# Optimization experiments

Measured on AMD Instinct MI355X. Metric: run time of the kernel, lower is better.

The kernel has to match this reference:

```python
import jax, jax.numpy as jnp
import numpy as np

# Gating config (matches init_kwargs)
N_GROUPS = 4        # n_expert_groups
TOPK_GROUPS = 2     # n_limited_groups
TOPK = 4            # n_activated_experts
ROUTE_SCALE = 1.0


def setup_inputs() -> dict:
    key = jax.random.key(0)
    ks = jax.random.split(key, 8)
    T, D, E, I = 2048, 1024, 16, 512
    s = 0.02  # init scale for sane numerics
    return {
        "x": jax.random.normal(ks[0], (T, D), jnp.float32),
        "gate_w": jax.random.normal(ks[1], (E, D), jnp.float32) * s,
        "w1": jax.random.normal(ks[2], (E, I, D), jnp.float32) * s,
        "w2": jax.random.normal(ks[3], (E, D, I), jnp.float32) * s,
        "w3": jax.random.normal(ks[4], (E, I, D), jnp.float32) * s,
        "ws1": jax.random.normal(ks[5], (I, D), jnp.float32) * s,
        "ws2": jax.random.normal(ks[6], (D, I), jnp.float32) * s,
        "ws3": jax.random.normal(ks[7], (I, D), jnp.float32) * s,
    }


def _gate(x, gate_w):
    # GateDeepSeekV3.forward: softmax scores, group-limited routing, top-k experts.
    T = x.shape[0]
    scores = jax.nn.softmax((x @ gate_w.T).astype(jnp.float32), axis=-1)  # [T, E]
    original_scores = scores
    E = scores.shape[-1]
    # group-limited routing: keep top `TOPK_GROUPS` groups by max score (bias is None)
    s = scores.reshape(T, N_GROUPS, E // N_GROUPS)
    group_scores = s.max(axis=-1)                                  # [T, G]
    _, gidx = jax.lax.top_k(group_scores, TOPK_GROUPS)             # [T, Gk]
    mask = jnp.zeros((T, N_GROUPS), scores.dtype).at[jnp.arange(T)[:, None], gidx].set(1.0)
    s = (s * mask[:, :, None]).reshape(T, E)
    _, indices = jax.lax.top_k(s, TOPK)                            # [T, topk]
    weights = jnp.take_along_axis(original_scores, indices, axis=1) * ROUTE_SCALE
    return weights.astype(x.dtype), indices


def reference(x, gate_w, w1, w2, w3, ws1, ws2, ws3):
    T, D = x.shape
    E = w1.shape[0]
    weights, indices = _gate(x, gate_w)
    # dense [T, E] combine weights (topk indices are unique per token)
    gate_dense = jnp.zeros((T, E), x.dtype).at[jnp.arange(T)[:, None], indices].add(weights)
    # routed experts: y_t = sum_e g[t,e] * W2_e (silu(W1_e x) * (W3_e x))
    h = jax.nn.silu(jnp.einsum('td,eid->tei', x, w1)) * jnp.einsum('td,eid->tei', x, w3)
    y = jnp.einsum('tei,te,edi->td', h, gate_dense, w2)
    # shared expert MLP over all tokens
    z = (jax.nn.silu(x @ ws1.T) * (x @ ws3.T)) @ ws2.T
    return y + z
```

## Files before the change

kernel.cpp:

```cpp
#include <hip/hip_runtime.h>
#include <hip/hip_bf16.h>
#include <math.h>

typedef float v4f __attribute__((ext_vector_type(4)));
typedef short v8s __attribute__((ext_vector_type(8)));

#define T_TOK   2048
#define DDIM    1024
#define NE      16
#define IDIM    512
#define S_ROUTED 8192
#define S_ALL   10240
#define MAXTILE 104

#define OFF_TOPKI    0u
#define OFF_TOPKW    32768u
#define OFF_PART     65536u
#define OFF_CBASE    69632u
#define OFF_SEGOFF   73728u
#define OFF_NTILES   74240u
#define OFF_TROW     74752u
#define OFF_TEND     75776u
#define OFF_TEXP     76800u
#define OFF_SLOTWT   81920u
#define OFF_S2T      114688u
#define OFF_SLOTOF   155648u
#define OFF_XBF      (1u<<20)
#define OFF_H        (8u<<20)
#define OFF_YP       (24u<<20)
#define OFF_W1BF     (24u<<20)
#define OFF_W3BF     (40u<<20)
#define OFF_W2BF     (56u<<20)
#define OFF_S1BF     (72u<<20)
#define OFF_S3BF     (73u<<20)
#define OFF_S2BF     (74u<<20)

__device__ __forceinline__ unsigned short f2bf(float f) {
    unsigned int u = __float_as_uint(f);
    unsigned int r = (u + 0x7fffu + ((u >> 16) & 1u)) >> 16;
    return (unsigned short)r;
}
__device__ __forceinline__ float bf2f(unsigned short s) {
    return __uint_as_float((unsigned)s << 16);
}
__device__ __forceinline__ unsigned cvt2(float lo, float hi) {
    unsigned r;
    asm("v_cvt_pk_bf16_f32 %0, %1, %2" : "=v"(r) : "v"(lo), "v"(hi));
    return r;
}

#define GLL16(gp, lp) __builtin_amdgcn_global_load_lds( \
    (__attribute__((address_space(1))) void*)(gp), \
    (__attribute__((address_space(3))) void*)(lp), 16, 0, 0)

__global__ __launch_bounds__(256) void wconv_kernel(
    const float* __restrict__ w1, const float* __restrict__ w3,
    const float* __restrict__ w2, const float* __restrict__ s1,
    const float* __restrict__ s3, const float* __restrict__ s2,
    unsigned short* __restrict__ o1, unsigned short* __restrict__ o3,
    unsigned short* __restrict__ o2, unsigned short* __restrict__ os1,
    unsigned short* __restrict__ os3, unsigned short* __restrict__ os2)
{
    const int BIG = 1048576;
    const int SMALL = 65536;
    const int total = 3 * BIG + 3 * SMALL;
    for (int i = blockIdx.x * 256 + threadIdx.x; i < total; i += gridDim.x * 256) {
        const float* s; unsigned short* d; int off;
        if (i < BIG)            { s = w1; d = o1;  off = i; }
        else if (i < 2 * BIG)   { s = w3; d = o3;  off = i - BIG; }
        else if (i < 3 * BIG)   { s = w2; d = o2;  off = i - 2 * BIG; }
        else {
            int k = i - 3 * BIG;
            if (k < SMALL)          { s = s1; d = os1; off = k; }
            else if (k < 2 * SMALL) { s = s3; d = os3; off = k - SMALL; }
            else                    { s = s2; d = os2; off = k - 2 * SMALL; }
        }
        float4 a = *(const float4*)(s + (size_t)off * 8);
        float4 b = *(const float4*)(s + (size_t)off * 8 + 4);
        uint4 p;
        p.x = cvt2(a.x, a.y); p.y = cvt2(a.z, a.w);
        p.z = cvt2(b.x, b.y); p.w = cvt2(b.z, b.w);
        *(uint4*)(d + (size_t)off * 8) = p;
    }
}

__global__ __launch_bounds__(256) void gate_kernel(
    const float* __restrict__ x, const float* __restrict__ gw,
    int* __restrict__ topki, float* __restrict__ topkw,
    unsigned short* __restrict__ xbf)
{
    int t = blockIdx.x;
    int tid = threadIdx.x, lane = tid & 63, wave = tid >> 6;
    const float4* xr = (const float4*)(x + (size_t)t * DDIM);
    float4 xv[4];
#pragma unroll
    for (int j = 0; j < 4; j++) xv[j] = xr[lane + 64 * j];

    __shared__ float sc[NE];
#pragma unroll
    for (int ee = 0; ee < 4; ee++) {
        int e = wave * 4 + ee;
        const float4* wr = (const float4*)(gw + (size_t)e * DDIM);
        float acc = 0.f;
#pragma unroll
        for (int j = 0; j < 4; j++) {
            float4 w = wr[lane + 64 * j];
            acc += xv[j].x * w.x + xv[j].y * w.y + xv[j].z * w.z + xv[j].w * w.w;
        }
#pragma unroll
        for (int off = 32; off; off >>= 1) acc += __shfl_down(acc, off, 64);
        if (lane == 0) sc[e] = acc;
    }
    if (wave == 0) {
#pragma unroll
        for (int j = 0; j < 4; j++) {
            int base = 4 * (lane + 64 * j);
            uint2 p;
            p.x = (unsigned)f2bf(xv[j].x) | ((unsigned)f2bf(xv[j].y) << 16);
            p.y = (unsigned)f2bf(xv[j].z) | ((unsigned)f2bf(xv[j].w) << 16);
            *(uint2*)(xbf + (size_t)t * DDIM + base) = p;
        }
    }
    __syncthreads();
    if (tid == 0) {
        float mx = sc[0];
#pragma unroll
        for (int e = 1; e < NE; e++) mx = fmaxf(mx, sc[e]);
        float sco[NE]; float sum = 0.f;
#pragma unroll
        for (int e = 0; e < NE; e++) { sco[e] = __expf(sc[e] - mx); sum += sco[e]; }
        float inv = 1.f / sum;
#pragma unroll
        for (int e = 0; e < NE; e++) sco[e] *= inv;
        float gs[4];
#pragma unroll
        for (int g = 0; g < 4; g++) {
            float m = sco[4 * g];
            m = fmaxf(m, sco[4 * g + 1]); m = fmaxf(m, sco[4 * g + 2]); m = fmaxf(m, sco[4 * g + 3]);
            gs[g] = m;
        }
        int g0 = 0;
        for (int g = 1; g < 4; g++) if (gs[g] > gs[g0]) g0 = g;
        int g1 = -1;
        for (int g = 0; g < 4; g++) { if (g == g0) continue; if (g1 < 0 || gs[g] > gs[g1]) g1 = g; }
        float ms[NE];
#pragma unroll
        for (int e = 0; e < NE; e++) {
            int g = e >> 2;
            ms[e] = (g == g0 || g == g1) ? sco[e] : 0.0f;
        }
        bool used[NE] = {false};
        for (int k = 0; k < 4; k++) {
            int best = -1;
            for (int e = 0; e < NE; e++) {
                if (used[e]) continue;
                if (best < 0 || ms[e] > ms[best]) best = e;
            }
            used[best] = true;
            topki[t * 4 + k] = best;
            topkw[t * 4 + k] = sco[best];
        }
    }
}

__global__ __launch_bounds__(256) void hist_kernel(
    const int* __restrict__ topki, int* __restrict__ part)
{
    __shared__ int cnt[16];
    int tid = threadIdx.x, b = blockIdx.x;
    if (tid < 16) cnt[tid] = 0;
    __syncthreads();
    int e = topki[b * 256 + tid];
    int lane = tid & 63;
#pragma unroll
    for (int e0 = 0; e0 < 16; e0++) {
        unsigned long long mask = __ballot(e == e0);
        if (lane == 0) atomicAdd(&cnt[e0], __popcll(mask));
    }
    __syncthreads();
    if (tid < 16) part[b * 16 + tid] = cnt[tid];
}

__global__ __launch_bounds__(256) void scan_kernel(
    const int* __restrict__ part, int* __restrict__ cbase, int* __restrict__ segoff,
    int* __restrict__ trow, int* __restrict__ tend, int* __restrict__ texp,
    int* __restrict__ ntp)
{
    int tid = threadIdx.x;
    __shared__ int tot[16];
    __shared__ int so[17];
    if (tid < 16) {
        int s = 0;
        for (int b = 0; b < 32; b++) s += part[b * 16 + tid];
        tot[tid] = s;
    }
    __syncthreads();
    if (tid == 0) {
        int off = 0;
        for (int e = 0; e < 16; e++) { so[e] = off; segoff[e] = off; off += tot[e]; }
        so[16] = off; segoff[16] = off; segoff[17] = off + T_TOK;
        int nt = 0;
        for (int e = 0; e < 17; e++) {
            int n = (e < 16) ? tot[e] : T_TOK;
            int base = (e < 16) ? so[e] : S_ROUTED;
            for (int m = 0; m < n; m += 128) {
                trow[nt] = base + m; tend[nt] = base + n; texp[nt] = e; nt++;
            }
        }
        *ntp = nt;
    }
    __syncthreads();
    if (tid < 16) {
        int run = so[tid];
        for (int b = 0; b < 32; b++) { cbase[b * 16 + tid] = run; run += part[b * 16 + tid]; }
    }
}

__global__ __launch_bounds__(256) void assign_kernel(
    const int* __restrict__ topki, const float* __restrict__ topkw,
    const int* __restrict__ cbase, int* __restrict__ s2t,
    float* __restrict__ slotwt, int* __restrict__ slotof)
{
    int b = blockIdx.x, tid = threadIdx.x;
    int i = b * 256 + tid;
    int e = topki[i];
    int lane = tid & 63, wave = tid >> 6;
    __shared__ int wcnt[4][16];
    int lrank = 0;
#pragma unroll
    for (int e0 = 0; e0 < 16; e0++) {
        unsigned long long mask = __ballot(e == e0);
        if (e == e0) lrank = __popcll(mask & ((1ull << lane) - 1ull));
        if (lane == 0) wcnt[wave][e0] = __popcll(mask);
    }
    __syncthreads();
    int pre = 0;
    for (int w = 0; w < wave; w++) pre += wcnt[w][e];
    int slot = cbase[b * 16 + e] + pre + lrank;
    int t = i >> 2;
    s2t[slot] = t;
    slotwt[slot] = topkw[i];
    slotof[i] = slot;
    if ((i & 3) == 0) s2t[S_ROUTED + t] = t;
}

#define G1_ISSUE(T, BUF) do {                                                  \
    _Pragma("unroll")                                                          \
    for (int j = 0; j < 4; j++)                                                \
        GLL16(asrc[j] + (T) * 64, (short*)As[BUF] + wave * 2048 + j * 512);    \
    _Pragma("unroll")                                                          \
    for (int j = 0; j < 4; j++)                                                \
        GLL16(bsrc[j] + (T) * 64, (short*)Bs[BUF] + wave * 512 + j * 2048);    \
} while (0)

#define G1_COMP(BUF) do {                                                      \
    const short* Ac = (const short*)As[BUF];                                   \
    const short* Bc = (const short*)Bs[BUF];                                   \
    _Pragma("unroll")                                                          \
    for (int ks = 0; ks < 2; ks++) {                                           \
        int kb = ks * 4 + mq;                                                  \
        v8s a[4], b[4];                                                        \
        _Pragma("unroll")                                                      \
        for (int mi = 0; mi < 4; mi++) {                                       \
            int R = wm * 64 + mi * 16 + nl;                                    \
            a[mi] = *(const v8s*)(Ac + R * 64 + ((kb ^ (nl & 7)) * 8));        \
        }                                                                      \
        _Pragma("unroll")                                                      \
        for (int ni = 0; ni < 4; ni++) {                                       \
            int S = (ni >> 1) * 64 + wn * 32 + (ni & 1) * 16 + nl;             \
            b[ni] = *(const v8s*)(Bc + S * 64 + ((kb ^ (nl & 7)) * 8));        \
        }                                                                      \
        _Pragma("unroll")                                                      \
        for (int mi = 0; mi < 4; mi++)                                         \
            _Pragma("unroll")                                                  \
            for (int ni = 0; ni < 4; ni++)                                     \
                acc[mi][ni] = __builtin_amdgcn_mfma_f32_16x16x32_bf16(         \
                    a[mi], b[ni], acc[mi][ni], 0, 0, 0);                       \
    }                                                                          \
} while (0)

__global__ __launch_bounds__(256, 2) void gemm1_kernel(
    const unsigned short* __restrict__ w1bf, const unsigned short* __restrict__ w3bf,
    const unsigned short* __restrict__ s1bf, const unsigned short* __restrict__ s3bf,
    const unsigned short* __restrict__ xbf,
    unsigned short* __restrict__ h, const float* __restrict__ slotwt,
    const int* __restrict__ s2t,
    const int* __restrict__ trow, const int* __restrict__ tend,
    const int* __restrict__ texp, const int* __restrict__ ntp)
{
    int bid = blockIdx.x;
    int tile = bid >> 3, ct = bid & 7;
    if (tile >= *ntp) return;
    int row0 = trow[tile], rend = tend[tile], e = texp[tile];
    int n0 = ct * 64;
    const unsigned short* B1 = (e < 16) ? (w1bf + (size_t)e * 524288) : s1bf;
    const unsigned short* B3 = (e < 16) ? (w3bf + (size_t)e * 524288) : s3bf;

    __shared__ __align__(16) short As[2][128 * 64];
    __shared__ __align__(16) short Bs[2][128 * 64];

    int tid = threadIdx.x;
    int lane = tid & 63, wave = tid >> 6;
    int wm = wave & 1, wn = wave >> 1;
    int mq = lane >> 4, nl = lane & 15;
    int rr = lane >> 3, s7 = lane & 7;
    int swz = (s7 ^ rr) * 8;

    const unsigned short* asrc[4];
#pragma unroll
    for (int j = 0; j < 4; j++)
        asrc[j] = xbf + (size_t)s2t[row0 + wave * 32 + j * 8 + rr] * DDIM + swz;

    const unsigned short* bsrc[4];
#pragma unroll
    for (int j = 0; j < 4; j++) {
        int R = wave * 8 + j * 32 + rr;
        const unsigned short* base = (R >> 6) ? B3 : B1;
        bsrc[j] = base + (size_t)(n0 + (R & 63)) * DDIM + swz;
    }

    v4f acc[4][4];
#pragma unroll
    for (int i = 0; i < 4; i++)
#pragma unroll
        for (int j = 0; j < 4; j++) acc[i][j] = (v4f)0.f;

    G1_ISSUE(0, 0);
    G1_ISSUE(1, 1);
    for (int ki = 0; ki < 15; ki++) {
        asm volatile("s_waitcnt vmcnt(8)" ::: "memory");
        __builtin_amdgcn_s_barrier();
        G1_COMP(ki & 1);
        __builtin_amdgcn_s_barrier();
        if (ki < 14) G1_ISSUE(ki + 2, ki & 1);
    }
    asm volatile("s_waitcnt vmcnt(0)" ::: "memory");
    __builtin_amdgcn_s_barrier();
    G1_COMP(1);

#pragma unroll
    for (int mi = 0; mi < 4; mi++) {
#pragma unroll
        for (int r = 0; r < 4; r++) {
            int srow = row0 + wm * 64 + mi * 16 + mq * 4 + r;
            if (srow < rend) {
                float g = (srow < S_ROUTED) ? slotwt[srow] : 1.0f;
#pragma unroll
                for (int ni = 0; ni < 2; ni++) {
                    float p1 = acc[mi][ni][r], p3 = acc[mi][ni + 2][r];
                    float sig = 1.f / (1.f + __expf(-p1));
                    h[(size_t)srow * IDIM + n0 + wn * 32 + ni * 16 + nl] = f2bf(p1 * sig * p3 * g);
                }
            }
        }
    }
}

#define G2_ISSUE(T, BUF) do {                                                  \
    _Pragma("unroll")                                                          \
    for (int j = 0; j < 4; j++)                                                \
        GLL16(asrc[j] + (T) * 64, (short*)As[BUF] + wave * 2048 + j * 512);    \
    _Pragma("unroll")                                                          \
    for (int j = 0; j < 4; j++)                                                \
        GLL16(bsrc[j] + (T) * 64, (short*)Bs[BUF] + wave * 512 + j * 2048);    \
} while (0)

#define G2_COMP(BUF) do {                                                      \
    const short* Ac = (const short*)As[BUF];                                   \
    const short* Bc = (const short*)Bs[BUF];                                   \
    _Pragma("unroll")                                                          \
    for (int ks = 0; ks < 2; ks++) {                                           \
        int kb = ks * 4 + mq;                                                  \
        v8s a[4], b[4];                                                        \
        _Pragma("unroll")                                                      \
        for (int mi = 0; mi < 4; mi++) {                                       \
            int R = wm * 64 + mi * 16 + nl;                                    \
            a[mi] = *(const v8s*)(Ac + R * 64 + ((kb ^ (nl & 7)) * 8));        \
        }                                                                      \
        _Pragma("unroll")                                                      \
        for (int ni = 0; ni < 4; ni++) {                                       \
            int S = wn * 64 + ni * 16 + nl;                                    \
            b[ni] = *(const v8s*)(Bc + S * 64 + ((kb ^ (nl & 7)) * 8));        \
        }                                                                      \
        _Pragma("unroll")                                                      \
        for (int mi = 0; mi < 4; mi++)                                         \
            _Pragma("unroll")                                                  \
            for (int ni = 0; ni < 4; ni++)                                     \
                acc[mi][ni] = __builtin_amdgcn_mfma_f32_16x16x32_bf16(         \
                    a[mi], b[ni], acc[mi][ni], 0, 0, 0);                       \
    }                                                                          \
} while (0)

__global__ __launch_bounds__(256, 2) void gemm2_kernel(
    const unsigned short* __restrict__ w2bf, const unsigned short* __restrict__ s2bf,
    const unsigned short* __restrict__ h, unsigned short* __restrict__ yp,
    const int* __restrict__ trow, const int* __restrict__ tend,
    const int* __restrict__ texp, const int* __restrict__ ntp)
{
    int bid = blockIdx.x;
    int tile = bid >> 3, ct = bid & 7;
    if (tile >= *ntp) return;
    int row0 = trow[tile], rend = tend[tile], e = texp[tile];
    int n0 = ct * 128;
    const unsigned short* B = ((e < 16) ? (w2bf + (size_t)e * 524288) : s2bf) + (size_t)n0 * IDIM;

    __shared__ __align__(16) short As[2][128 * 64];
    __shared__ __align__(16) short Bs[2][128 * 64];

    int tid = threadIdx.x;
    int lane = tid & 63, wave = tid >> 6;
    int wm = wave & 1, wn = wave >> 1;
    int mq = lane >> 4, nl = lane & 15;
    int rr = lane >> 3, s7 = lane & 7;
    int swz = (s7 ^ rr) * 8;

    const unsigned short* asrc[4];
#pragma unroll
    for (int j = 0; j < 4; j++)
        asrc[j] = h + (size_t)(row0 + wave * 32 + j * 8 + rr) * IDIM + swz;

    const unsigned short* bsrc[4];
#pragma unroll
    for (int j = 0; j < 4; j++) {
        int R = wave * 8 + j * 32 + rr;
        bsrc[j] = B + (size_t)R * IDIM + swz;
    }

    v4f acc[4][4];
#pragma unroll
    for (int i = 0; i < 4; i++)
#pragma unroll
        for (int j = 0; j < 4; j++) acc[i][j] = (v4f)0.f;

    G2_ISSUE(0, 0);
    G2_ISSUE(1, 1);
    for (int ki = 0; ki < 7; ki++) {
        asm volatile("s_waitcnt vmcnt(8)" ::: "memory");
        __builtin_amdgcn_s_barrier();
        G2_COMP(ki & 1);
        __builtin_amdgcn_s_barrier();
        if (ki < 6) G2_ISSUE(ki + 2, ki & 1);
    }
    asm volatile("s_waitcnt vmcnt(0)" ::: "memory");
    __builtin_amdgcn_s_barrier();
    G2_COMP(1);

#pragma unroll
    for (int mi = 0; mi < 4; mi++) {
#pragma unroll
        for (int r = 0; r < 4; r++) {
            int srow = row0 + wm * 64 + mi * 16 + mq * 4 + r;
            if (srow < rend) {
                unsigned short* yrow = yp + ((size_t)srow << 10) + n0 + wn * 64 + nl;
#pragma unroll
                for (int ni = 0; ni < 4; ni++)
                    yrow[ni * 16] = f2bf(acc[mi][ni][r]);
            }
        }
    }
}

__global__ __launch_bounds__(256) void combine_kernel(
    const unsigned short* __restrict__ yp, const int* __restrict__ slotof,
    float* __restrict__ out)
{
    int t = blockIdx.x;
    int c = threadIdx.x * 4;
    int s0 = slotof[t * 4 + 0], s1 = slotof[t * 4 + 1];
    int s2 = slotof[t * 4 + 2], s3 = slotof[t * 4 + 3];
    ushort4 v  = *(const ushort4*)(yp + (((size_t)(S_ROUTED + t)) << 10) + c);
    ushort4 a0 = *(const ushort4*)(yp + (((size_t)s0) << 10) + c);
    ushort4 a1 = *(const ushort4*)(yp + (((size_t)s1) << 10) + c);
    ushort4 a2 = *(const ushort4*)(yp + (((size_t)s2) << 10) + c);
    ushort4 a3 = *(const ushort4*)(yp + (((size_t)s3) << 10) + c);
    float4 o;
    o.x = bf2f(v.x) + bf2f(a0.x) + bf2f(a1.x) + bf2f(a2.x) + bf2f(a3.x);
    o.y = bf2f(v.y) + bf2f(a0.y) + bf2f(a1.y) + bf2f(a2.y) + bf2f(a3.y);
    o.z = bf2f(v.z) + bf2f(a0.z) + bf2f(a1.z) + bf2f(a2.z) + bf2f(a3.z);
    o.w = bf2f(v.w) + bf2f(a0.w) + bf2f(a1.w) + bf2f(a2.w) + bf2f(a3.w);
    *(float4*)(out + (((size_t)t) << 10) + c) = o;
}

extern "C" void kernel_launch(void* const* d_in, const int* in_sizes, int n_in,
                              void* d_out, int out_size, void* d_ws, size_t ws_size,
                              hipStream_t stream) {
    const float* x    = (const float*)d_in[0];
    const float* gw   = (const float*)d_in[1];
    const float* w1   = (const float*)d_in[2];
    const float* w2   = (const float*)d_in[3];
    const float* w3   = (const float*)d_in[4];
    const float* wsh1 = (const float*)d_in[5];
    const float* wsh2 = (const float*)d_in[6];
    const float* wsh3 = (const float*)d_in[7];
    float* out = (float*)d_out;

    char* ws = (char*)d_ws;
    int*   topki  = (int*)(ws + OFF_TOPKI);
    float* topkw  = (float*)(ws + OFF_TOPKW);
    int*   part   = (int*)(ws + OFF_PART);
    int*   cbase  = (int*)(ws + OFF_CBASE);
    int*   segoff = (int*)(ws + OFF_SEGOFF);
    int*   ntp    = (int*)(ws + OFF_NTILES);
    int*   trow   = (int*)(ws + OFF_TROW);
    int*   tend   = (int*)(ws + OFF_TEND);
    int*   texp   = (int*)(ws + OFF_TEXP);
    float* slotwt = (float*)(ws + OFF_SLOTWT);
    int*   s2t    = (int*)(ws + OFF_S2T);
    int*   slotof = (int*)(ws + OFF_SLOTOF);
    unsigned short* xbf  = (unsigned short*)(ws + OFF_XBF);
    unsigned short* h    = (unsigned short*)(ws + OFF_H);
    unsigned short* yp   = (unsigned short*)(ws + OFF_YP);
    unsigned short* w1bf = (unsigned short*)(ws + OFF_W1BF);
    unsigned short* w3bf = (unsigned short*)(ws + OFF_W3BF);
    unsigned short* w2bf = (unsigned short*)(ws + OFF_W2BF);
    unsigned short* s1bf = (unsigned short*)(ws + OFF_S1BF);
    unsigned short* s3bf = (unsigned short*)(ws + OFF_S3BF);
    unsigned short* s2bf = (unsigned short*)(ws + OFF_S2BF);

    wconv_kernel<<<4096, 256, 0, stream>>>(w1, w3, w2, wsh1, wsh3, wsh2,
                                           w1bf, w3bf, w2bf, s1bf, s3bf, s2bf);
    gate_kernel<<<T_TOK, 256, 0, stream>>>(x, gw, topki, topkw, xbf);
    hist_kernel<<<32, 256, 0, stream>>>(topki, part);
    scan_kernel<<<1, 256, 0, stream>>>(part, cbase, segoff, trow, tend, texp, ntp);
    assign_kernel<<<32, 256, 0, stream>>>(topki, topkw, cbase, s2t, slotwt, slotof);
    gemm1_kernel<<<MAXTILE * 8, 256, 0, stream>>>(w1bf, w3bf, s1bf, s3bf, xbf, h, slotwt, s2t,
                                                  trow, tend, texp, ntp);
    gemm2_kernel<<<MAXTILE * 8, 256, 0, stream>>>(w2bf, s2bf, h, yp, trow, tend, texp, ntp);
    combine_kernel<<<T_TOK, 256, 0, stream>>>(yp, slotof, out);
}
```

Baseline: 242.4 us.

## Fuse weight conversion into gate kernel and triple-buffer both expert GEMMs

Merges the fp32→bf16 weight conversion loop into the gate kernel, which removes one launch and lets the conversion share blocks with the routing work. Both grouped GEMM kernels move from double to triple LDS buffering, keeping three K-tiles in flight. Wait counts are adjusted per iteration and the peeled tail is folded into the loop. The larger LDS footprint (96KB per block) drops occupancy hint to one block per CU, trading latency hiding via occupancy for deeper prefetch.

```diff
diff --git a/kernel.cpp b/kernel.cpp
--- a/kernel.cpp
+++ b/kernel.cpp
@@ -53,41 +53,16 @@
     (__attribute__((address_space(1))) void*)(gp), \
     (__attribute__((address_space(3))) void*)(lp), 16, 0, 0)
 
-__global__ __launch_bounds__(256) void wconv_kernel(
+__global__ __launch_bounds__(256) void gate_kernel(
+    const float* __restrict__ x, const float* __restrict__ gw,
+    int* __restrict__ topki, float* __restrict__ topkw,
+    unsigned short* __restrict__ xbf,
     const float* __restrict__ w1, const float* __restrict__ w3,
     const float* __restrict__ w2, const float* __restrict__ s1,
     const float* __restrict__ s3, const float* __restrict__ s2,
     unsigned short* __restrict__ o1, unsigned short* __restrict__ o3,
     unsigned short* __restrict__ o2, unsigned short* __restrict__ os1,
     unsigned short* __restrict__ os3, unsigned short* __restrict__ os2)
-{
-    const int BIG = 1048576;
-    const int SMALL = 65536;
-    const int total = 3 * BIG + 3 * SMALL;
-    for (int i = blockIdx.x * 256 + threadIdx.x; i < total; i += gridDim.x * 256) {
-        const float* s; unsigned short* d; int off;
-        if (i < BIG)            { s = w1; d = o1;  off = i; }
-        else if (i < 2 * BIG)   { s = w3; d = o3;  off = i - BIG; }
-        else if (i < 3 * BIG)   { s = w2; d = o2;  off = i - 2 * BIG; }
-        else {
-            int k = i - 3 * BIG;
-            if (k < SMALL)          { s = s1; d = os1; off = k; }
-            else if (k < 2 * SMALL) { s = s3; d = os3; off = k - SMALL; }
-            else                    { s = s2; d = os2; off = k - 2 * SMALL; }
-        }
-        float4 a = *(const float4*)(s + (size_t)off * 8);
-        float4 b = *(const float4*)(s + (size_t)off * 8 + 4);
-        uint4 p;
-        p.x = cvt2(a.x, a.y); p.y = cvt2(a.z, a.w);
-        p.z = cvt2(b.x, b.y); p.w = cvt2(b.z, b.w);
-        *(uint4*)(d + (size_t)off * 8) = p;
-    }
-}
-
-__global__ __launch_bounds__(256) void gate_kernel(
-    const float* __restrict__ x, const float* __restrict__ gw,
-    int* __restrict__ topki, float* __restrict__ topkw,
-    unsigned short* __restrict__ xbf)
 {
     int t = blockIdx.x;
     int tid = threadIdx.x, lane = tid & 63, wave = tid >> 6;
@@ -160,6 +135,27 @@
             topki[t * 4 + k] = best;
             topkw[t * 4 + k] = sco[best];
         }
+    }
+    const int BIG = 1048576;
+    const int SMALL = 65536;
+    const int total = 3 * BIG + 3 * SMALL;
+    for (int i = blockIdx.x * 256 + tid; i < total; i += gridDim.x * 256) {
+        const float* s; unsigned short* d; int off;
+        if (i < BIG)            { s = w1; d = o1;  off = i; }
+        else if (i < 2 * BIG)   { s = w3; d = o3;  off = i - BIG; }
+        else if (i < 3 * BIG)   { s = w2; d = o2;  off = i - 2 * BIG; }
+        else {
+            int k = i - 3 * BIG;
+            if (k < SMALL)          { s = s1; d = os1; off = k; }
+            else if (k < 2 * SMALL) { s = s3; d = os3; off = k - SMALL; }
+            else                    { s = s2; d = os2; off = k - 2 * SMALL; }
+        }
+        float4 a = *(const float4*)(s + (size_t)off * 8);
+        float4 b = *(const float4*)(s + (size_t)off * 8 + 4);
+        uint4 p;
+        p.x = cvt2(a.x, a.y); p.y = cvt2(a.z, a.w);
+        p.z = cvt2(b.x, b.y); p.w = cvt2(b.z, b.w);
+        *(uint4*)(d + (size_t)off * 8) = p;
     }
 }
 
@@ -279,7 +275,7 @@
     }                                                                          \
 } while (0)
 
-__global__ __launch_bounds__(256, 2) void gemm1_kernel(
+__global__ __launch_bounds__(256, 1) void gemm1_kernel(
     const unsigned short* __restrict__ w1bf, const unsigned short* __restrict__ w3bf,
     const unsigned short* __restrict__ s1bf, const unsigned short* __restrict__ s3bf,
     const unsigned short* __restrict__ xbf,
@@ -296,8 +292,8 @@
     const unsigned short* B1 = (e < 16) ? (w1bf + (size_t)e * 524288) : s1bf;
     const unsigned short* B3 = (e < 16) ? (w3bf + (size_t)e * 524288) : s3bf;
 
-    __shared__ __align__(16) short As[2][128 * 64];
-    __shared__ __align__(16) short Bs[2][128 * 64];
+    __shared__ __align__(16) short As[3][128 * 64];
+    __shared__ __align__(16) short Bs[3][128 * 64];
 
     int tid = threadIdx.x;
     int lane = tid & 63, wave = tid >> 6;
@@ -327,16 +323,17 @@
 
     G1_ISSUE(0, 0);
     G1_ISSUE(1, 1);
-    for (int ki = 0; ki < 15; ki++) {
-        asm volatile("s_waitcnt vmcnt(8)" ::: "memory");
+    G1_ISSUE(2, 2);
+    for (int ki = 0; ki < 16; ki++) {
+        if (ki < 14)      asm volatile("s_waitcnt vmcnt(16)" ::: "memory");
+        else if (ki == 14) asm volatile("s_waitcnt vmcnt(8)" ::: "memory");
+        else               asm volatile("s_waitcnt vmcnt(0)" ::: "memory");
         __builtin_amdgcn_s_barrier();
-        G1_COMP(ki & 1);
+        int buf = ki % 3;
+        G1_COMP(buf);
         __builtin_amdgcn_s_barrier();
-        if (ki < 14) G1_ISSUE(ki + 2, ki & 1);
-    }
-    asm volatile("s_waitcnt vmcnt(0)" ::: "memory");
-    __builtin_amdgcn_s_barrier();
-    G1_COMP(1);
+        if (ki < 13) G1_ISSUE(ki + 3, buf);
+    }
 
 #pragma unroll
     for (int mi = 0; mi < 4; mi++) {
@@ -391,7 +388,7 @@
     }                                                                          \
 } while (0)
 
-__global__ __launch_bounds__(256, 2) void gemm2_kernel(
+__global__ __launch_bounds__(256, 1) void gemm2_kernel(
     const unsigned short* __restrict__ w2bf, const unsigned short* __restrict__ s2bf,
     const unsigned short* __restrict__ h, unsigned short* __restrict__ yp,
     const int* __restrict__ trow, const int* __restrict__ tend,
@@ -404,8 +401,8 @@
     int n0 = ct * 128;
     const unsigned short* B = ((e < 16) ? (w2bf + (size_t)e * 524288) : s2bf) + (size_t)n0 * IDIM;
 
-    __shared__ __align__(16) short As[2][128 * 64];
-    __shared__ __align__(16) short Bs[2][128 * 64];
+    __shared__ __align__(16) short As[3][128 * 64];
+    __shared__ __align__(16) short Bs[3][128 * 64];
 
     int tid = threadIdx.x;
     int lane = tid & 63, wave = tid >> 6;
@@ -434,16 +431,17 @@
 
     G2_ISSUE(0, 0);
     G2_ISSUE(1, 1);
-    for (int ki = 0; ki < 7; ki++) {
-        asm volatile("s_waitcnt vmcnt(8)" ::: "memory");
+    G2_ISSUE(2, 2);
+    for (int ki = 0; ki < 8; ki++) {
+        if (ki < 6)       asm volatile("s_waitcnt vmcnt(16)" ::: "memory");
+        else if (ki == 6) asm volatile("s_waitcnt vmcnt(8)" ::: "memory");
+        else              asm volatile("s_waitcnt vmcnt(0)" ::: "memory");
         __builtin_amdgcn_s_barrier();
-        G2_COMP(ki & 1);
+        int buf = ki % 3;
+        G2_COMP(buf);
         __builtin_amdgcn_s_barrier();
-        if (ki < 6) G2_ISSUE(ki + 2, ki & 1);
-    }
-    asm volatile("s_waitcnt vmcnt(0)" ::: "memory");
-    __builtin_amdgcn_s_barrier();
-    G2_COMP(1);
+        if (ki < 5) G2_ISSUE(ki + 3, buf);
+    }
 
 #pragma unroll
     for (int mi = 0; mi < 4; mi++) {
@@ -517,9 +515,9 @@
     unsigned short* s3bf = (unsigned short*)(ws + OFF_S3BF);
     unsigned short* s2bf = (unsigned short*)(ws + OFF_S2BF);
 
-    wconv_kernel<<<4096, 256, 0, stream>>>(w1, w3, w2, wsh1, wsh3, wsh2,
+    gate_kernel<<<T_TOK, 256, 0, stream>>>(x, gw, topki, topkw, xbf,
+                                           w1, w3, w2, wsh1, wsh3, wsh2,
                                            w1bf, w3bf, w2bf, s1bf, s3bf, s2bf);
-    gate_kernel<<<T_TOK, 256, 0, stream>>>(x, gw, topki, topkw, xbf);
     hist_kernel<<<32, 256, 0, stream>>>(topki, part);
     scan_kernel<<<1, 256, 0, stream>>>(part, cbase, segoff, trow, tend, texp, ntp);
     assign_kernel<<<32, 256, 0, stream>>>(topki, topkw, cbase, s2t, slotwt, slotof);
```

Result: slower. 262.5 us (+8.3%).
